# Performance work log

Hardware: AMD Instinct MI355X
Metric: run time of the kernel (lower is better)

## Reference

```python
import jax, jax.numpy as jnp
import numpy as np

B, N, NODE_DIM = 8, 128, 64
L, RES_DIM = 512, 1024
CG, CP = 128, 128
NUM_GNN_STEPS = 3
HID = CG + CP // 2  # interaction hidden = 192


def setup_inputs() -> dict:
    key = jax.random.key(0)
    ks = jax.random.split(key, 20)
    a = (jax.random.uniform(ks[0], (B, N, N)) < 0.05).astype(jnp.float32)
    adj = jnp.clip(a + jnp.swapaxes(a, 1, 2), 0.0, 1.0)
    adj = adj * (1.0 - jnp.eye(N, dtype=jnp.float32))
    nodes = jax.random.normal(ks[1], (B, N, NODE_DIM), dtype=jnp.float32)
    prot = jax.random.normal(ks[2], (B, L, RES_DIM), dtype=jnp.float32)
    s = 0.02
    inp = {
        "adj_mats": adj, "nodes": nodes, "protein_sequences": prot,
        "Wn": jax.random.normal(ks[3], (NODE_DIM, CG)) * s, "bn": jnp.zeros((CG,)),
        "Wg": jax.random.normal(ks[4], (CG, CG)) * s, "bg": jnp.zeros((CG,)),
        "Wr": jax.random.normal(ks[5], (RES_DIM, CP)) * s, "br": jnp.zeros((CP,)),
        "Wa": jax.random.normal(ks[6], (CG + CP, 1)) * s, "ba": jnp.zeros((1,)),
        "W1": jax.random.normal(ks[7], (CG + CP, HID)) * s, "b1": jnp.zeros((HID,)),
        "W2": jax.random.normal(ks[8], (HID, CG)) * s, "b2": jnp.zeros((CG,)),
        "Wo": jax.random.normal(ks[9], (CG, 1)) * s, "bo": jnp.zeros((1,)),
    }
    return inp


def reference(adj_mats, nodes, protein_sequences,
              Wn, bn, Wg, bg, Wr, br, Wa, ba, W1, b1, W2, b2, Wo, bo):
    # node compression: [B,N,CG]
    h = nodes @ Wn + bn
    deg = jnp.clip(jnp.sum(adj_mats, axis=-1), 1.0, None)        # [B,N]
    norm = deg ** -0.5                                           # [B,N]
    for i in range(NUM_GNN_STEPS):
        m = jnp.einsum('bij,bjc->bic', adj_mats, h * norm[..., None])
        h = (m * norm[..., None]) @ Wg + bg
        h = jnp.tanh(h) if i == NUM_GNN_STEPS - 1 else jax.nn.relu(h)
    # residue compression: [B,L,CP]
    r = protein_sequences @ Wr + br
    # MergeSnE1: all-pairs broadcast concat -> [B, N*L, CG+CP]
    cat = jnp.concatenate([
        jnp.broadcast_to(h[:, :, None, :], (B, N, L, CG)),
        jnp.broadcast_to(r[:, None, :, :], (B, N, L, CP)),
    ], axis=-1).reshape(B, N * L, CG + CP)
    # attention: Linear -> Softmax over last dim (size 1 => all ones, faithful)
    attn = jax.nn.softmax(cat @ Wa + ba, axis=-1)                # [B,N*L,1]
    inter = jax.nn.relu(cat @ W1 + b1) @ W2 + b2                 # [B,N*L,CG]
    weighted_sum = jnp.sum(attn * inter, axis=1)                 # [B,CG]
    return weighted_sum @ Wo + bo                                # [B,1]
```

## Files before the change

kernel.cpp:

```cpp
#include <hip/hip_runtime.h>
#include <hip/hip_bf16.h>

#define BB 8
#define NN 128
#define ND 64
#define LL 512
#define RD 1024
#define CG 128
#define HID 192

typedef __attribute__((ext_vector_type(8))) short short8;
typedef __attribute__((ext_vector_type(4))) float f32x4;

__device__ __forceinline__ unsigned short f2bf(float x) {
    return __bfloat16_as_ushort(__float2bfloat16(x));
}
__device__ __forceinline__ float bf2f(unsigned short h) {
    unsigned u = ((unsigned)h) << 16;
    return __builtin_bit_cast(float, u);
}
__device__ __forceinline__ float fast_tanh(float x) {
    float e = __expf(2.0f * x);
    return 1.0f - 2.0f * __builtin_amdgcn_rcpf(e + 1.0f);
}
#define MFMA __builtin_amdgcn_mfma_f32_16x16x32_bf16

__global__ __launch_bounds__(512, 1) void k_gnn(
    const float* __restrict__ adj, const float* __restrict__ nodes,
    const float* __restrict__ Wn, const float* __restrict__ bn,
    const float* __restrict__ br, const float* __restrict__ W1,
    const float* __restrict__ b1, const float* __restrict__ Wg,
    const float* __restrict__ bg,
    unsigned short* __restrict__ hW1b)
{
    __shared__ unsigned short hT[NN][136];
    __shared__ unsigned short mbuf[NN][72];
    __shared__ unsigned short WgT[NN][136];
    __shared__ unsigned short W1T[HID][136];
    __shared__ float snorm[NN];
    __shared__ float b1cL[HID];
    __shared__ float sbg[NN];
    int t = threadIdx.x, blk = blockIdx.x;
    int w = t >> 6, l = t & 63, lr = l & 15, ks = l >> 4, lk = ks * 8;
    const float* W1b = W1 + CG * HID;
    int b = blk;
    int i0 = w * 16;

    {
        float* dscr = (float*)&mbuf[0][0];
        int row = t >> 2, q4 = t & 3;
        const float* ar = adj + ((size_t)b * NN + row) * NN + q4 * 32;
        float d = 0.f;
        #pragma unroll
        for (int c4 = 0; c4 < 8; ++c4) {
            float4 p = *(const float4*)(ar + c4 * 4);
            d += (p.x + p.y) + (p.z + p.w);
        }
        dscr[row * 4 + q4] = d;
        __syncthreads();
        if (t < NN) {
            snorm[t] = rsqrtf(fmaxf(dscr[t*4] + dscr[t*4+1] + dscr[t*4+2] + dscr[t*4+3], 1.f));
        } else if (t < 320) {
            int j = t - 128;
            float s = b1[j];
            #pragma unroll 8
            for (int m = 0; m < CG; ++m)
                s = fmaf(br[m], W1b[(size_t)m * HID + j], s);
            b1cL[j] = s;
        } else if (t < 448) {
            sbg[t - 320] = bg[t - 320];
        }
        __syncthreads();
    }

    unsigned short* WnT = &mbuf[0][0];
    #pragma unroll
    for (int q = 0; q < 16; ++q) {
        int e = t + 512 * q;
        int c = e & 127, k = e >> 7;
        WnT[c * 72 + k] = f2bf(Wn[(size_t)k * CG + c]);
    }
    #pragma unroll
    for (int q = 0; q < 32; ++q) {
        int e = t + 512 * q;
        int c = e & 127, j = e >> 7;
        WgT[c][j] = f2bf(Wg[(size_t)j * CG + c]);
    }
    #pragma unroll
    for (int q = 0; q < 32; ++q) {
        int e = t + 512 * q;
        int jj = e & 127, k = e >> 7;
        W1T[jj][k] = f2bf(W1[(size_t)k * HID + jj]);
    }
    #pragma unroll
    for (int q = 0; q < 16; ++q) {
        int e = t + 512 * q;
        int jj = 128 + (e & 63), k = e >> 6;
        W1T[jj][k] = f2bf(W1[(size_t)k * HID + jj]);
    }

    short8 af[4];
    {
        float ni = snorm[i0 + lr];
        const float* ar = adj + ((size_t)b * NN + i0 + lr) * NN;
        #pragma unroll
        for (int kk = 0; kk < 4; ++kk) {
            int kb = kk * 32 + lk;
            float4 p0 = *(const float4*)(ar + kb);
            float4 p1 = *(const float4*)(ar + kb + 4);
            unsigned short u[8];
            u[0] = f2bf(p0.x * ni * snorm[kb+0]); u[1] = f2bf(p0.y * ni * snorm[kb+1]);
            u[2] = f2bf(p0.z * ni * snorm[kb+2]); u[3] = f2bf(p0.w * ni * snorm[kb+3]);
            u[4] = f2bf(p1.x * ni * snorm[kb+4]); u[5] = f2bf(p1.y * ni * snorm[kb+5]);
            u[6] = f2bf(p1.z * ni * snorm[kb+6]); u[7] = f2bf(p1.w * ni * snorm[kb+7]);
            af[kk] = *(const short8*)u;
        }
    }
    short8 bnod[2];
    #pragma unroll
    for (int kk = 0; kk < 2; ++kk) {
        const float* np = nodes + ((size_t)b * NN + i0 + lr) * ND + kk * 32 + lk;
        float4 q0 = *(const float4*)np;
        float4 q1 = *(const float4*)(np + 4);
        unsigned short u[8];
        u[0]=f2bf(q0.x); u[1]=f2bf(q0.y); u[2]=f2bf(q0.z); u[3]=f2bf(q0.w);
        u[4]=f2bf(q1.x); u[5]=f2bf(q1.y); u[6]=f2bf(q1.z); u[7]=f2bf(q1.w);
        bnod[kk] = *(const short8*)u;
    }
    __syncthreads();

    #pragma unroll
    for (int ct = 0; ct < 8; ++ct) {
        f32x4 d = {0.f, 0.f, 0.f, 0.f};
        #pragma unroll
        for (int kk = 0; kk < 2; ++kk) {
            short8 afw = *(const short8*)(WnT + (ct * 16 + lr) * 72 + kk * 32 + lk);
            d = MFMA(afw, bnod[kk], d, 0, 0, 0);
        }
        #pragma unroll
        for (int i = 0; i < 4; ++i)
            hT[ct * 16 + ks * 4 + i][i0 + lr] = f2bf(d[i] + bn[ct * 16 + ks * 4 + i]);
    }
    __syncthreads();

    for (int s = 0; s < 3; ++s) {
        f32x4 acc8[8];
        #pragma unroll
        for (int ct = 0; ct < 8; ++ct) acc8[ct] = (f32x4){0.f, 0.f, 0.f, 0.f};
        #pragma unroll
        for (int hf = 0; hf < 2; ++hf) {
            #pragma unroll
            for (int jt = 0; jt < 4; ++jt) {
                int jg = hf * 64 + jt * 16;
                f32x4 d = {0.f, 0.f, 0.f, 0.f};
                #pragma unroll
                for (int kk = 0; kk < 4; ++kk) {
                    short8 bf = *(const short8*)(&hT[jg + lr][kk * 32 + lk]);
                    d = MFMA(af[kk], bf, d, 0, 0, 0);
                }
                #pragma unroll
                for (int i = 0; i < 4; ++i)
                    mbuf[i0 + ks * 4 + i][jt * 16 + lr] = f2bf(d[i]);
            }
            short8 bm[2];
            #pragma unroll
            for (int kk = 0; kk < 2; ++kk)
                bm[kk] = *(const short8*)(&mbuf[i0 + lr][kk * 32 + lk]);
            #pragma unroll
            for (int ct = 0; ct < 8; ++ct) {
                #pragma unroll
                for (int kk = 0; kk < 2; ++kk) {
                    short8 wf = *(const short8*)(&WgT[ct * 16 + lr][hf * 64 + kk * 32 + lk]);
                    if (s < 2)
                        acc8[ct] = MFMA(wf, bm[kk], acc8[ct], 0, 0, 0);
                    else
                        acc8[ct] = MFMA(bm[kk], wf, acc8[ct], 0, 0, 0);
                }
            }
        }
        __syncthreads();
        if (s < 2) {
            #pragma unroll
            for (int ct = 0; ct < 8; ++ct)
                #pragma unroll
                for (int i = 0; i < 4; ++i)
                    hT[ct * 16 + ks * 4 + i][i0 + lr] =
                        f2bf(fmaxf(acc8[ct][i] + sbg[ct * 16 + ks * 4 + i], 0.f));
        } else {
            #pragma unroll
            for (int ct = 0; ct < 8; ++ct)
                #pragma unroll
                for (int i = 0; i < 4; ++i)
                    hT[i0 + ks * 4 + i][ct * 16 + lr] =
                        f2bf(fast_tanh(acc8[ct][i] + sbg[ct * 16 + lr]));
        }
        __syncthreads();
    }

    {
        short8 bh[4];
        #pragma unroll
        for (int kk = 0; kk < 4; ++kk)
            bh[kk] = *(const short8*)(&hT[i0 + lr][kk * 32 + lk]);
        #pragma unroll
        for (int jjt = 0; jjt < 12; ++jjt) {
            f32x4 d = {0.f, 0.f, 0.f, 0.f};
            #pragma unroll
            for (int kk = 0; kk < 4; ++kk) {
                short8 wf = *(const short8*)(&W1T[jjt * 16 + lr][kk * 32 + lk]);
                d = MFMA(wf, bh[kk], d, 0, 0, 0);
            }
            #pragma unroll
            for (int i = 0; i < 4; ++i) {
                int jj = jjt * 16 + ks * 4 + i;
                hW1b[(size_t)b * HID * NN + jj * NN + i0 + lr] = f2bf(d[i] + b1cL[jj]);
            }
        }
    }
}

__global__ __launch_bounds__(512, 1) void k_weights(
    const float* __restrict__ Wr, const float* __restrict__ W1,
    const float* __restrict__ W2, const float* __restrict__ b2,
    const float* __restrict__ Wo, const float* __restrict__ bo,
    unsigned short* __restrict__ WcT, float* __restrict__ vbuf,
    float* __restrict__ out)
{
    __shared__ unsigned short W1T[HID][136];
    int t = threadIdx.x, blk = blockIdx.x;
    int w = t >> 6, l = t & 63, lr = l & 15, ks = l >> 4, lk = ks * 8;

    if (blk == 16) {
        if (t < HID) {
            float s = 0.f;
            #pragma unroll 8
            for (int k = 0; k < CG; ++k) s = fmaf(W2[t * CG + k], Wo[k], s);
            vbuf[t] = s;
        }
        if (t < BB) {
            float s = 0.f;
            for (int k = 0; k < CG; ++k) s = fmaf(b2[k], Wo[k], s);
            out[t] = (float)(NN * LL) * s + bo[0];
        }
        return;
    }
    int r0 = blk * 64;
    #pragma unroll
    for (int q = 0; q < 48; ++q) {
        int e = t + 512 * q;
        int m = e / HID, c = e % HID;
        W1T[c][m] = f2bf(W1[(size_t)(CG + m) * HID + c]);
    }
    int rt = w & 3, jh = w >> 2;
    short8 awr[4];
    #pragma unroll
    for (int kk = 0; kk < 4; ++kk) {
        const float* wp = Wr + (size_t)(r0 + rt * 16 + lr) * CG + kk * 32 + lk;
        float4 q0 = *(const float4*)wp;
        float4 q1 = *(const float4*)(wp + 4);
        unsigned short u[8];
        u[0]=f2bf(q0.x); u[1]=f2bf(q0.y); u[2]=f2bf(q0.z); u[3]=f2bf(q0.w);
        u[4]=f2bf(q1.x); u[5]=f2bf(q1.y); u[6]=f2bf(q1.z); u[7]=f2bf(q1.w);
        awr[kk] = *(const short8*)u;
    }
    __syncthreads();
    #pragma unroll
    for (int jt6 = 0; jt6 < 6; ++jt6) {
        int jt = jh * 6 + jt6;
        f32x4 d = {0.f, 0.f, 0.f, 0.f};
        #pragma unroll
        for (int kk = 0; kk < 4; ++kk) {
            short8 bf = *(const short8*)(&W1T[jt * 16 + lr][kk * 32 + lk]);
            d = MFMA(awr[kk], bf, d, 0, 0, 0);
        }
        unsigned short u[4];
        #pragma unroll
        for (int i = 0; i < 4; ++i) u[i] = f2bf(d[i]);
        *(uint2*)(WcT + (size_t)(jt * 16 + lr) * RD + r0 + rt * 16 + ks * 4) = *(uint2*)u;
    }
}

__global__ __launch_bounds__(512, 4) void k_gemm(
    const float* __restrict__ prot, const unsigned short* __restrict__ WcT,
    const unsigned short* __restrict__ hW1b, const float* __restrict__ vbuf,
    float* __restrict__ out)
{
    __shared__ unsigned short aT[16 * 1032];
    __shared__ unsigned short h1[HID * 136];
    __shared__ float pbuf[2 * 16 * 192];
    __shared__ float sred[8];
    int t = threadIdx.x, blk = blockIdx.x;
    int b = blk >> 5, lc = blk & 31;
    int w = t >> 6, l = t & 63, lr = l & 15, ks = l >> 4, lk = ks * 8;
    int w2 = w >> 2, wj = w & 3;

    #pragma unroll
    for (int q = 0; q < 4; ++q) {
        int e = t + 512 * q;
        int row = e >> 7;
        int c8 = (e & 127) * 8;
        const float* pr = prot + ((size_t)(b * LL + lc * 16 + row)) * RD + c8;
        float4 p0 = *(const float4*)pr;
        float4 p1 = *(const float4*)(pr + 4);
        unsigned short u[8];
        u[0]=f2bf(p0.x); u[1]=f2bf(p0.y); u[2]=f2bf(p0.z); u[3]=f2bf(p0.w);
        u[4]=f2bf(p1.x); u[5]=f2bf(p1.y); u[6]=f2bf(p1.z); u[7]=f2bf(p1.w);
        *(short8*)(aT + row * 1032 + c8) = *(const short8*)u;
    }
    #pragma unroll
    for (int q = 0; q < 6; ++q) {
        int u8 = t + 512 * q;
        int row = u8 >> 4;
        int n8 = (u8 & 15) * 8;
        short8 v = *(const short8*)(hW1b + (size_t)b * HID * NN + row * NN + n8);
        *(short8*)(h1 + row * 136 + n8) = v;
    }
    float v0 = vbuf[wj * 48 + lr];
    float v1 = vbuf[wj * 48 + 16 + lr];
    float v2 = vbuf[wj * 48 + 32 + lr];
    __syncthreads();

    f32x4 a0 = {0.f,0.f,0.f,0.f}, a1 = a0, a2 = a0;
    {
        const unsigned short* ap = aT + lr * 1032 + w2 * 512 + lk;
        const unsigned short* bp = WcT + (size_t)(wj * 48 + lr) * RD + w2 * 512 + lk;
        #pragma unroll 4
        for (int k0 = 0; k0 < 512; k0 += 32) {
            short8 av = *(const short8*)(ap + k0);
            short8 b0 = *(const short8*)(bp + k0);
            short8 b1 = *(const short8*)(bp + 16 * RD + k0);
            short8 b2 = *(const short8*)(bp + 32 * RD + k0);
            a0 = MFMA(av, b0, a0, 0, 0, 0);
            a1 = MFMA(av, b1, a1, 0, 0, 0);
            a2 = MFMA(av, b2, a2, 0, 0, 0);
        }
    }
    #pragma unroll
    for (int i = 0; i < 4; ++i) {
        int r = ks * 4 + i;
        pbuf[(w2 * 16 + r) * 192 + wj * 48 + lr]      = a0[i];
        pbuf[(w2 * 16 + r) * 192 + wj * 48 + 16 + lr] = a1[i];
        pbuf[(w2 * 16 + r) * 192 + wj * 48 + 32 + lr] = a2[i];
    }
    __syncthreads();
    float rw0[4], rw1[4], rw2[4];
    #pragma unroll
    for (int i = 0; i < 4; ++i) {
        int r = ks * 4 + i;
        rw0[i] = pbuf[r * 192 + wj*48 + lr]      + pbuf[(16 + r) * 192 + wj*48 + lr];
        rw1[i] = pbuf[r * 192 + wj*48 + 16 + lr] + pbuf[(16 + r) * 192 + wj*48 + 16 + lr];
        rw2[i] = pbuf[r * 192 + wj*48 + 32 + lr] + pbuf[(16 + r) * 192 + wj*48 + 32 + lr];
    }

    const unsigned short* h0p = h1 + (wj * 48 + lr) * 136 + w2 * 64;
    const unsigned short* h1p = h0p + 16 * 136;
    const unsigned short* h2p = h0p + 32 * 136;
    float s = 0.f;
    #pragma unroll 2
    for (int n0 = 0; n0 < 64; n0 += 4) {
        unsigned short e0[4], e1[4], e2[4];
        *(uint2*)e0 = *(const uint2*)(h0p + n0);
        *(uint2*)e1 = *(const uint2*)(h1p + n0);
        *(uint2*)e2 = *(const uint2*)(h2p + n0);
        #pragma unroll
        for (int q = 0; q < 4; ++q) {
            float hh0 = bf2f(e0[q]), hh1 = bf2f(e1[q]), hh2 = bf2f(e2[q]);
            #pragma unroll
            for (int i = 0; i < 4; ++i) {
                s = fmaf(v0, fmaxf(rw0[i] + hh0, 0.f), s);
                s = fmaf(v1, fmaxf(rw1[i] + hh1, 0.f), s);
                s = fmaf(v2, fmaxf(rw2[i] + hh2, 0.f), s);
            }
        }
    }
    for (int off = 32; off; off >>= 1) s += __shfl_down(s, off);
    if (l == 0) sred[w] = s;
    __syncthreads();
    if (t == 0) {
        float tot = ((sred[0] + sred[1]) + (sred[2] + sred[3]))
                  + ((sred[4] + sred[5]) + (sred[6] + sred[7]));
        atomicAdd(&out[b], tot);
    }
}

extern "C" void kernel_launch(void* const* d_in, const int* in_sizes, int n_in,
                              void* d_out, int out_size, void* d_ws, size_t ws_size,
                              hipStream_t stream)
{
    const float* adj   = (const float*)d_in[0];
    const float* nodes = (const float*)d_in[1];
    const float* prot  = (const float*)d_in[2];
    const float* Wn    = (const float*)d_in[3];
    const float* bn    = (const float*)d_in[4];
    const float* Wg    = (const float*)d_in[5];
    const float* bg    = (const float*)d_in[6];
    const float* Wr    = (const float*)d_in[7];
    const float* br    = (const float*)d_in[8];
    const float* W1    = (const float*)d_in[11];
    const float* b1    = (const float*)d_in[12];
    const float* W2    = (const float*)d_in[13];
    const float* b2    = (const float*)d_in[14];
    const float* Wo    = (const float*)d_in[15];
    const float* bo    = (const float*)d_in[16];

    float* ws     = (float*)d_ws;
    float* vbuf   = ws;
    unsigned short* hW1b = (unsigned short*)(ws + 192);
    unsigned short* WcT  = hW1b + (size_t)BB * HID * NN;
    float* out    = (float*)d_out;

    hipLaunchKernelGGL(k_gnn, dim3(8), dim3(512), 0, stream,
                       adj, nodes, Wn, bn, br, W1, b1, Wg, bg, hW1b);
    hipLaunchKernelGGL(k_weights, dim3(17), dim3(512), 0, stream,
                       Wr, W1, W2, b2, Wo, bo, WcT, vbuf, out);
    hipLaunchKernelGGL(k_gemm, dim3(256), dim3(512), 0, stream,
                       prot, WcT, hW1b, vbuf, out);
}
```

Before: 61.87 us.

## Precompute transposed bf16 weights and folded bias in a new prep kernel ahead of GNN

Moves the weight transposition and bf16 conversion of Wg, W1 and Wn, plus the folded b1+br·W1 bias, out of the 8-block GNN kernel. They now run in a new 25-block prep kernel that also absorbs the former k_weights work. The GNN kernel then copies pre-transposed bf16 weights with vectorized 16-byte loads instead of doing strided scalar fp32 gathers on only 8 blocks. This reorders the stages so the weight work runs before the GNN, adding a dependency and global round-trips through workspace.

```diff
diff --git a/kernel.cpp b/kernel.cpp
--- a/kernel.cpp
+++ b/kernel.cpp
@@ -25,12 +25,124 @@
 }
 #define MFMA __builtin_amdgcn_mfma_f32_16x16x32_bf16
 
+__global__ __launch_bounds__(512, 1) void k1(
+    const float* __restrict__ Wr, const float* __restrict__ br,
+    const float* __restrict__ W1, const float* __restrict__ b1,
+    const float* __restrict__ Wg, const float* __restrict__ Wn,
+    const float* __restrict__ W2, const float* __restrict__ b2,
+    const float* __restrict__ Wo, const float* __restrict__ bo,
+    unsigned short* __restrict__ WcT, float* __restrict__ vbuf,
+    float* __restrict__ b1cg, float* __restrict__ out,
+    unsigned short* __restrict__ WgTg, unsigned short* __restrict__ W1Tg,
+    unsigned short* __restrict__ WnTg)
+{
+    __shared__ unsigned short W1T[HID][136];
+    int t = threadIdx.x, blk = blockIdx.x;
+    int w = t >> 6, l = t & 63, lr = l & 15, ks = l >> 4, lk = ks * 8;
+    const float* W1b = W1 + CG * HID;
+
+    if (blk < 16) {
+        int r0 = blk * 64;
+        #pragma unroll
+        for (int q = 0; q < 48; ++q) {
+            int e = t + 512 * q;
+            int m = e / HID, c = e % HID;
+            W1T[c][m] = f2bf(W1[(size_t)(CG + m) * HID + c]);
+        }
+        int rt = w & 3, jh = w >> 2;
+        short8 awr[4];
+        #pragma unroll
+        for (int kk = 0; kk < 4; ++kk) {
+            const float* wp = Wr + (size_t)(r0 + rt * 16 + lr) * CG + kk * 32 + lk;
+            float4 q0 = *(const float4*)wp;
+            float4 q1 = *(const float4*)(wp + 4);
+            unsigned short u[8];
+            u[0]=f2bf(q0.x); u[1]=f2bf(q0.y); u[2]=f2bf(q0.z); u[3]=f2bf(q0.w);
+            u[4]=f2bf(q1.x); u[5]=f2bf(q1.y); u[6]=f2bf(q1.z); u[7]=f2bf(q1.w);
+            awr[kk] = *(const short8*)u;
+        }
+        __syncthreads();
+        #pragma unroll
+        for (int jt6 = 0; jt6 < 6; ++jt6) {
+            int jt = jh * 6 + jt6;
+            f32x4 d = {0.f, 0.f, 0.f, 0.f};
+            #pragma unroll
+            for (int kk = 0; kk < 4; ++kk) {
+                short8 bf = *(const short8*)(&W1T[jt * 16 + lr][kk * 32 + lk]);
+                d = MFMA(awr[kk], bf, d, 0, 0, 0);
+            }
+            unsigned short u[4];
+            #pragma unroll
+            for (int i = 0; i < 4; ++i) u[i] = f2bf(d[i]);
+            *(uint2*)(WcT + (size_t)(jt * 16 + lr) * RD + r0 + rt * 16 + ks * 4) = *(uint2*)u;
+        }
+        return;
+    }
+    if (blk == 16) {
+        if (t < HID) {
+            float s = 0.f;
+            #pragma unroll 8
+            for (int k = 0; k < CG; ++k) s = fmaf(W2[t * CG + k], Wo[k], s);
+            vbuf[t] = s;
+        }
+        if (t < BB) {
+            float s = 0.f;
+            for (int k = 0; k < CG; ++k) s = fmaf(b2[k], Wo[k], s);
+            out[t] = (float)(NN * LL) * s + bo[0];
+        }
+        if (t >= 192 && t < 384) {
+            int j = t - 192;
+            float s = b1[j];
+            #pragma unroll 8
+            for (int m = 0; m < CG; ++m)
+                s = fmaf(br[m], W1b[(size_t)m * HID + j], s);
+            b1cg[j] = s;
+        }
+        return;
+    }
+    if (blk < 21) {
+        int c = (blk - 17) * 32 + (t >> 4);
+        int j8 = (t & 15) * 8;
+        unsigned short u[8];
+        #pragma unroll
+        for (int q = 0; q < 8; ++q)
+            u[q] = f2bf(Wg[(size_t)(j8 + q) * CG + c]);
+        *(short8*)(WgTg + (size_t)c * CG + j8) = *(const short8*)u;
+        return;
+    }
+    if (blk < 24) {
+        int jj0 = (blk - 21) * 64;
+        #pragma unroll
+        for (int qq = 0; qq < 2; ++qq) {
+            int u8 = t + 512 * qq;
+            int jj = jj0 + (u8 >> 4);
+            int k8 = (u8 & 15) * 8;
+            unsigned short u[8];
+            #pragma unroll
+            for (int q = 0; q < 8; ++q)
+                u[q] = f2bf(W1[(size_t)(k8 + q) * HID + jj]);
+            *(short8*)(W1Tg + (size_t)jj * CG + k8) = *(const short8*)u;
+        }
+        return;
+    }
+    #pragma unroll
+    for (int qq = 0; qq < 2; ++qq) {
+        int u8 = t + 512 * qq;
+        int c = u8 >> 3;
+        int k8 = (u8 & 7) * 8;
+        unsigned short u[8];
+        #pragma unroll
+        for (int q = 0; q < 8; ++q)
+            u[q] = f2bf(Wn[(size_t)(k8 + q) * CG + c]);
+        *(short8*)(WnTg + (size_t)c * ND + k8) = *(const short8*)u;
+    }
+}
+
 __global__ __launch_bounds__(512, 1) void k_gnn(
     const float* __restrict__ adj, const float* __restrict__ nodes,
-    const float* __restrict__ Wn, const float* __restrict__ bn,
-    const float* __restrict__ br, const float* __restrict__ W1,
-    const float* __restrict__ b1, const float* __restrict__ Wg,
-    const float* __restrict__ bg,
+    const unsigned short* __restrict__ WnTg, const float* __restrict__ bn,
+    const unsigned short* __restrict__ WgTg, const float* __restrict__ bg,
+    const unsigned short* __restrict__ W1Tg, const float* __restrict__ b1cg,
     unsigned short* __restrict__ hW1b)
 {
     __shared__ unsigned short hT[NN][136];
@@ -42,7 +154,6 @@
     __shared__ float sbg[NN];
     int t = threadIdx.x, blk = blockIdx.x;
     int w = t >> 6, l = t & 63, lr = l & 15, ks = l >> 4, lk = ks * 8;
-    const float* W1b = W1 + CG * HID;
     int b = blk;
     int i0 = w * 16;
 
@@ -61,12 +172,7 @@
         if (t < NN) {
             snorm[t] = rsqrtf(fmaxf(dscr[t*4] + dscr[t*4+1] + dscr[t*4+2] + dscr[t*4+3], 1.f));
         } else if (t < 320) {
-            int j = t - 128;
-            float s = b1[j];
-            #pragma unroll 8
-            for (int m = 0; m < CG; ++m)
-                s = fmaf(br[m], W1b[(size_t)m * HID + j], s);
-            b1cL[j] = s;
+            b1cL[t - 128] = b1cg[t - 128];
         } else if (t < 448) {
             sbg[t - 320] = bg[t - 320];
         }
@@ -75,28 +181,22 @@
 
     unsigned short* WnT = &mbuf[0][0];
     #pragma unroll
-    for (int q = 0; q < 16; ++q) {
-        int e = t + 512 * q;
-        int c = e & 127, k = e >> 7;
-        WnT[c * 72 + k] = f2bf(Wn[(size_t)k * CG + c]);
-    }
-    #pragma unroll
-    for (int q = 0; q < 32; ++q) {
-        int e = t + 512 * q;
-        int c = e & 127, j = e >> 7;
-        WgT[c][j] = f2bf(Wg[(size_t)j * CG + c]);
-    }
-    #pragma unroll
-    for (int q = 0; q < 32; ++q) {
-        int e = t + 512 * q;
-        int jj = e & 127, k = e >> 7;
-        W1T[jj][k] = f2bf(W1[(size_t)k * HID + jj]);
-    }
-    #pragma unroll
-    for (int q = 0; q < 16; ++q) {
-        int e = t + 512 * q;
-        int jj = 128 + (e & 63), k = e >> 6;
-        W1T[jj][k] = f2bf(W1[(size_t)k * HID + jj]);
+    for (int qq = 0; qq < 2; ++qq) {
+        int u8 = t + 512 * qq;
+        int c = u8 >> 3, k8 = (u8 & 7) * 8;
+        *(short8*)(WnT + c * 72 + k8) = *(const short8*)(WnTg + (size_t)c * ND + k8);
+    }
+    #pragma unroll
+    for (int qq = 0; qq < 4; ++qq) {
+        int u8 = t + 512 * qq;
+        int c = u8 >> 4, j8 = (u8 & 15) * 8;
+        *(short8*)(&WgT[c][j8]) = *(const short8*)(WgTg + (size_t)c * CG + j8);
+    }
+    #pragma unroll
+    for (int qq = 0; qq < 6; ++qq) {
+        int u8 = t + 512 * qq;
+        int jj = u8 >> 4, k8 = (u8 & 15) * 8;
+        *(short8*)(&W1T[jj][k8]) = *(const short8*)(W1Tg + (size_t)jj * CG + k8);
     }
 
     short8 af[4];
@@ -216,67 +316,6 @@
                 hW1b[(size_t)b * HID * NN + jj * NN + i0 + lr] = f2bf(d[i] + b1cL[jj]);
             }
         }
-    }
-}
-
-__global__ __launch_bounds__(512, 1) void k_weights(
-    const float* __restrict__ Wr, const float* __restrict__ W1,
-    const float* __restrict__ W2, const float* __restrict__ b2,
-    const float* __restrict__ Wo, const float* __restrict__ bo,
-    unsigned short* __restrict__ WcT, float* __restrict__ vbuf,
-    float* __restrict__ out)
-{
-    __shared__ unsigned short W1T[HID][136];
-    int t = threadIdx.x, blk = blockIdx.x;
-    int w = t >> 6, l = t & 63, lr = l & 15, ks = l >> 4, lk = ks * 8;
-
-    if (blk == 16) {
-        if (t < HID) {
-            float s = 0.f;
-            #pragma unroll 8
-            for (int k = 0; k < CG; ++k) s = fmaf(W2[t * CG + k], Wo[k], s);
-            vbuf[t] = s;
-        }
-        if (t < BB) {
-            float s = 0.f;
-            for (int k = 0; k < CG; ++k) s = fmaf(b2[k], Wo[k], s);
-            out[t] = (float)(NN * LL) * s + bo[0];
-        }
-        return;
-    }
-    int r0 = blk * 64;
-    #pragma unroll
-    for (int q = 0; q < 48; ++q) {
-        int e = t + 512 * q;
-        int m = e / HID, c = e % HID;
-        W1T[c][m] = f2bf(W1[(size_t)(CG + m) * HID + c]);
-    }
-    int rt = w & 3, jh = w >> 2;
-    short8 awr[4];
-    #pragma unroll
-    for (int kk = 0; kk < 4; ++kk) {
-        const float* wp = Wr + (size_t)(r0 + rt * 16 + lr) * CG + kk * 32 + lk;
-        float4 q0 = *(const float4*)wp;
-        float4 q1 = *(const float4*)(wp + 4);
-        unsigned short u[8];
-        u[0]=f2bf(q0.x); u[1]=f2bf(q0.y); u[2]=f2bf(q0.z); u[3]=f2bf(q0.w);
-        u[4]=f2bf(q1.x); u[5]=f2bf(q1.y); u[6]=f2bf(q1.z); u[7]=f2bf(q1.w);
-        awr[kk] = *(const short8*)u;
-    }
-    __syncthreads();
-    #pragma unroll
-    for (int jt6 = 0; jt6 < 6; ++jt6) {
-        int jt = jh * 6 + jt6;
-        f32x4 d = {0.f, 0.f, 0.f, 0.f};
-        #pragma unroll
-        for (int kk = 0; kk < 4; ++kk) {
-            short8 bf = *(const short8*)(&W1T[jt * 16 + lr][kk * 32 + lk]);
-            d = MFMA(awr[kk], bf, d, 0, 0, 0);
-        }
-        unsigned short u[4];
-        #pragma unroll
-        for (int i = 0; i < 4; ++i) u[i] = f2bf(d[i]);
-        *(uint2*)(WcT + (size_t)(jt * 16 + lr) * RD + r0 + rt * 16 + ks * 4) = *(uint2*)u;
     }
 }
 
@@ -405,14 +444,19 @@
 
     float* ws     = (float*)d_ws;
     float* vbuf   = ws;
-    unsigned short* hW1b = (unsigned short*)(ws + 192);
+    float* b1cg   = ws + 192;
+    unsigned short* hW1b = (unsigned short*)(ws + 384);
     unsigned short* WcT  = hW1b + (size_t)BB * HID * NN;
+    unsigned short* WgTg = WcT + (size_t)HID * RD;
+    unsigned short* W1Tg = WgTg + CG * CG;
+    unsigned short* WnTg = W1Tg + HID * CG;
     float* out    = (float*)d_out;
 
+    hipLaunchKernelGGL(k1, dim3(25), dim3(512), 0, stream,
+                       Wr, br, W1, b1, Wg, Wn, W2, b2, Wo, bo,
+                       WcT, vbuf, b1cg, out, WgTg, W1Tg, WnTg);
     hipLaunchKernelGGL(k_gnn, dim3(8), dim3(512), 0, stream,
-                       adj, nodes, Wn, bn, br, W1, b1, Wg, bg, hW1b);
-    hipLaunchKernelGGL(k_weights, dim3(17), dim3(512), 0, stream,
-                       Wr, W1, W2, b2, Wo, bo, WcT, vbuf, out);
+                       adj, nodes, WnTg, bn, WgTg, bg, W1Tg, b1cg, hW1b);
     hipLaunchKernelGGL(k_gemm, dim3(256), dim3(512), 0, stream,
                        prot, WcT, hW1b, vbuf, out);
 }
```

Result: faster. 56.69 us (-8.4%).
